# Kernel tuning notes

Hardware: AMD Instinct MI355X
Metric: run time of the kernel (lower is better)

The kernel has to match this reference:

```python
import jax, jax.numpy as jnp
import numpy as np

B, S, HID = 1, 1024, 4096
H, D = 32, 128
KB, NUM_SLOTS, KB_IDX = 2048, 2, 0
TOPK = 100
THETA = 10000.0
KB_SCALE = 100.0
NEG = -1e9


def _rope(x, pos):
    # x: [B,H,S,D], pos: [B,S]
    inv = 1.0 / (THETA ** (jnp.arange(0, D, 2, dtype=jnp.float32) / D))
    freqs = pos[..., None].astype(jnp.float32) * inv          # [B,S,D/2]
    emb = jnp.concatenate([freqs, freqs], -1)                  # [B,S,D]
    cos = jnp.cos(emb)[:, None]                                # [B,1,S,D]
    sin = jnp.sin(emb)[:, None]
    x1, x2 = jnp.split(x, 2, -1)
    rot = jnp.concatenate([-x2, x1], -1)
    return x * cos + rot * sin


def setup_inputs() -> dict:
    key = jax.random.key(0)
    ks = jax.random.split(key, 8)
    hidden_states = jax.random.normal(ks[0], (B, S, HID), jnp.float32)
    # standard additive causal mask (0 on allowed, large negative above diagonal)
    causal = jnp.tril(jnp.ones((S, S), bool))
    attention_mask = jnp.where(causal, 0.0, NEG).astype(jnp.float32)[None, None]
    position_ids = jnp.arange(S, dtype=jnp.int64 if jax.config.jax_enable_x64 else jnp.int32)[None].astype(jnp.int32)
    kb_keys = jax.random.normal(ks[1], (KB, NUM_SLOTS * HID), jnp.float32)
    kb_values = jax.random.normal(ks[2], (KB, NUM_SLOTS * HID), jnp.float32)
    std = 0.02
    Wq = jax.random.normal(ks[3], (HID, HID), jnp.float32) * std
    Wq2 = jax.random.normal(ks[4], (HID, HID), jnp.float32) * std
    Wk = jax.random.normal(ks[5], (HID, HID), jnp.float32) * std
    Wv = jax.random.normal(ks[6], (HID, HID), jnp.float32) * std
    Wo = jax.random.normal(ks[7], (HID, HID), jnp.float32) * std
    score_shift = jnp.zeros((H, 1), jnp.float32) - 3.0
    return dict(hidden_states=hidden_states, attention_mask=attention_mask,
                position_ids=position_ids, kb_keys=kb_keys, kb_values=kb_values,
                Wq=Wq, Wq2=Wq2, Wk=Wk, Wv=Wv, Wo=Wo, score_shift=score_shift)


def reference(hidden_states, attention_mask, position_ids, kb_keys, kb_values,
              Wq, Wq2, Wk, Wv, Wo, score_shift):
    b, s, _ = hidden_states.shape
    heads = lambda x: x.reshape(b, s, H, D).transpose(0, 2, 1, 3)
    q = heads(hidden_states @ Wq.T)
    q2 = heads(hidden_states @ Wq2.T)
    k = heads(hidden_states @ Wk.T)
    v = heads(hidden_states @ Wv.T)
    q = _rope(q, position_ids)
    k = _rope(k, position_ids)
    scale = 1.0 / jnp.sqrt(jnp.asarray(D, jnp.float32))

    # ---- KB branch (2-dim kb_kvs, layer_idx % kb_layer_frequency == 0) ----
    kbk = kb_keys.reshape(KB, NUM_SLOTS, HID)[:, KB_IDX].reshape(KB, H, D).transpose(1, 0, 2)  # [H,KB,D]
    kbv = kb_values.reshape(KB, NUM_SLOTS, HID)[:, KB_IDX].reshape(KB, H, D).transpose(1, 0, 2)
    kbk = jnp.broadcast_to(kbk[None], (b, H, KB, D))
    kbv = jnp.broadcast_to(kbv[None], (b, H, KB, D))

    # dynamic_sparsify: top-k pruning of KB entries by summed q2-scores
    aw2_full = jnp.einsum('bhqd,bhkd->bhqk', q2, kbk) * scale     # [b,H,S,KB]
    kb_scores = jax.lax.stop_gradient(aw2_full.sum((1, 2)))       # [b,KB]
    _, top_idx = jax.lax.top_k(kb_scores, TOPK)                   # [b,TOPK]
    gather = jax.vmap(lambda a, i: a[:, i])                        # [H,KB,D],[TOPK]->[H,TOPK,D]
    kbk_t = gather(kbk, top_idx)
    kbv_t = gather(kbv, top_idx)

    keys = jnp.concatenate([kbk_t, k], 2)                         # [b,H,TOPK+S,D]
    vals = jnp.concatenate([kbv_t, v], 2)

    aw = jnp.einsum('bhqd,bhkd->bhqk', q, keys) * scale           # [b,H,S,TOPK+S]

    # sep_query_head: KB logits use q2, per-head score_shift, log scale-factor correction
    aw2 = jnp.einsum('bhqd,bhkd->bhqk', q2, kbk_t) * scale        # [b,H,S,TOPK]
    aw2 = aw2 + score_shift.reshape(1, H, 1, 1)
    aw2 = aw2 - jnp.log(jnp.asarray(TOPK, jnp.float32)) + jnp.log(jnp.asarray(KB_SCALE, jnp.float32))
    aw = jnp.concatenate([aw2, aw[..., TOPK:]], -1)

    # mask: KB columns fully visible (no fully-padded rows in causal mask)
    kb_mask = jnp.zeros((b, 1, s, TOPK), attention_mask.dtype)
    mask = jnp.concatenate([kb_mask, attention_mask], -1)
    probs = jax.nn.softmax((aw + mask).astype(jnp.float32), -1).astype(q.dtype)

    out = jnp.einsum('bhqk,bhkd->bhqd', probs, vals)
    out = out.transpose(0, 2, 1, 3).reshape(b, s, HID)
    return out @ Wo.T
```

## Files before the change

kernel.cpp:

```cpp
#include <hip/hip_runtime.h>
#include <hip/hip_bf16.h>
#include <math.h>

typedef __hip_bfloat16 bf16_t;
typedef __attribute__((ext_vector_type(8))) short short8;
typedef __attribute__((ext_vector_type(4))) float f32x4;

#define S_LEN 1024
#define HID   4096
#define NH    32
#define HD    128
#define KB_N  2048
#define TOPK  100
#define SCALE 0.08838834764831845f

typedef const __attribute__((address_space(1))) void* gptr_t;
typedef __attribute__((address_space(3))) void* lptr_t;

#define VM8 asm volatile("s_waitcnt vmcnt(8)" ::: "memory")
#define VM4 asm volatile("s_waitcnt vmcnt(4)" ::: "memory")
#define VM0 asm volatile("s_waitcnt vmcnt(0)" ::: "memory")

__global__ void k0_zero(float* __restrict__ out, float* __restrict__ hssum) {
  int tid = threadIdx.x;
  if (blockIdx.x < 4096) {
    float4 z = {0.f, 0.f, 0.f, 0.f};
    *(float4*)(out + ((size_t)blockIdx.x * 256 + tid) * 4) = z;
  } else {
    float4 z = {0.f, 0.f, 0.f, 0.f};
    *(float4*)(hssum + tid * 4) = z;
    *(float4*)(hssum + 1024 + tid * 4) = z;
    *(float4*)(hssum + 2048 + tid * 4) = z;
    *(float4*)(hssum + 3072 + tid * 4) = z;
  }
}

__global__ void kw_conv(const float* __restrict__ Wq, const float* __restrict__ Wq2,
                        const float* __restrict__ Wk, const float* __restrict__ Wv,
                        const float* __restrict__ Wo,
                        bf16_t* __restrict__ Wcat, bf16_t* __restrict__ Wob) {
  int w = blockIdx.y;
  const float* src = (w == 0) ? Wq : (w == 1) ? Wq2 : (w == 2) ? Wk : (w == 3) ? Wv : Wo;
  bf16_t* dst = (w < 4) ? (Wcat + (size_t)w * 16777216) : Wob;
  size_t i = ((size_t)blockIdx.x * 256 + threadIdx.x) * 4;
  float4 f = *(const float4*)(src + i);
  union { bf16_t h[4]; uint2 u; } p;
  p.h[0] = __float2bfloat16(f.x); p.h[1] = __float2bfloat16(f.y);
  p.h[2] = __float2bfloat16(f.z); p.h[3] = __float2bfloat16(f.w);
  *(uint2*)(dst + i) = p.u;
}

__global__ void k1_convert(const float* __restrict__ hs, bf16_t* __restrict__ hsb) {
  size_t i = ((size_t)blockIdx.x * 256 + threadIdx.x) * 4;
  float4 f = *(const float4*)(hs + i);
  union { bf16_t h[4]; uint2 u; } p;
  p.h[0] = __float2bfloat16(f.x); p.h[1] = __float2bfloat16(f.y);
  p.h[2] = __float2bfloat16(f.z); p.h[3] = __float2bfloat16(f.w);
  *(uint2*)(hsb + i) = p.u;
}

__global__ void k1_colsum(const float* __restrict__ hs, float* __restrict__ hssum) {
  int col = blockIdx.x * 256 + threadIdx.x;
  int r0 = blockIdx.y * 64;
  float acc = 0.f;
#pragma unroll 8
  for (int r = 0; r < 64; r++) acc += hs[(size_t)(r0 + r) * HID + col];
  atomicAdd(hssum + col, acc);
}

__global__ void k2_q2sum(const float* __restrict__ W,
                         const float* __restrict__ hssum,
                         float* __restrict__ q2sum) {
  int wave = threadIdx.x >> 6, lane = threadIdx.x & 63;
  int row = blockIdx.x * 4 + wave;
  const float4* wr = (const float4*)(W + (size_t)row * HID);
  const float4* xr = (const float4*)hssum;
  float acc = 0.f;
#pragma unroll
  for (int it = 0; it < 16; it++) {
    float4 a = wr[it * 64 + lane];
    float4 b = xr[it * 64 + lane];
    acc += a.x * b.x + a.y * b.y + a.z * b.z + a.w * b.w;
  }
#pragma unroll
  for (int off = 32; off > 0; off >>= 1) acc += __shfl_xor(acc, off, 64);
  if (lane == 0) q2sum[row] = acc;
}

__global__ void k3_kbscore(const float* __restrict__ kbk,
                           const float* __restrict__ q2sum,
                           float* __restrict__ scores) {
  int wave = threadIdx.x >> 6, lane = threadIdx.x & 63;
  int row = blockIdx.x * 4 + wave;
  const float4* kr = (const float4*)(kbk + (size_t)row * 8192);
  const float4* xr = (const float4*)q2sum;
  float acc = 0.f;
#pragma unroll
  for (int it = 0; it < 16; it++) {
    float4 a = kr[it * 64 + lane];
    float4 b = xr[it * 64 + lane];
    acc += a.x * b.x + a.y * b.y + a.z * b.z + a.w * b.w;
  }
#pragma unroll
  for (int off = 32; off > 0; off >>= 1) acc += __shfl_xor(acc, off, 64);
  if (lane == 0) scores[row] = acc * SCALE;
}

__global__ void k4_topk(const float* __restrict__ scores, int* __restrict__ tidx) {
  int lane = threadIdx.x;
  float v[32];
#pragma unroll
  for (int i = 0; i < 32; i++) v[i] = scores[i * 64 + lane];
  for (int t = 0; t < TOPK; t++) {
    float bm = -INFINITY; int bi = 0x7fffffff;
#pragma unroll
    for (int i = 0; i < 32; i++) {
      if (v[i] > bm) { bm = v[i]; bi = i * 64 + lane; }
    }
#pragma unroll
    for (int off = 32; off > 0; off >>= 1) {
      float ov = __shfl_xor(bm, off, 64);
      int   oi = __shfl_xor(bi, off, 64);
      if (ov > bm || (ov == bm && oi < bi)) { bm = ov; bi = oi; }
    }
    if (lane == 0) tidx[t] = bi;
    if ((bi & 63) == lane) {
      int slot = bi >> 6;
#pragma unroll
      for (int i = 0; i < 32; i++) if (i == slot) v[i] = -INFINITY;
    }
  }
}

__global__ void k5_gather(const float* __restrict__ kbk, const float* __restrict__ kbv,
                          const int* __restrict__ tidx,
                          bf16_t* __restrict__ kbkt, bf16_t* __restrict__ kbvt) {
  int j = blockIdx.x;
  int tid = threadIdx.x;
  if (j < TOPK) {
    size_t src = (size_t)tidx[j] * 8192;
#pragma unroll
    for (int r = 0; r < 4; r++) {
      int i = (tid + r * 256) * 4;
      float4 a = *(const float4*)(kbk + src + i);
      float4 b = *(const float4*)(kbv + src + i);
      union { bf16_t h[4]; uint2 u; } pa, pb;
      pa.h[0] = __float2bfloat16(a.x); pa.h[1] = __float2bfloat16(a.y);
      pa.h[2] = __float2bfloat16(a.z); pa.h[3] = __float2bfloat16(a.w);
      pb.h[0] = __float2bfloat16(b.x); pb.h[1] = __float2bfloat16(b.y);
      pb.h[2] = __float2bfloat16(b.z); pb.h[3] = __float2bfloat16(b.w);
      *(uint2*)(kbkt + (size_t)j * HID + i) = pa.u;
      *(uint2*)(kbvt + (size_t)j * HID + i) = pb.u;
    }
  } else {
    uint2 z; z.x = 0u; z.y = 0u;
#pragma unroll
    for (int r = 0; r < 4; r++) {
      int i = (tid + r * 256) * 4;
      *(uint2*)(kbkt + (size_t)j * HID + i) = z;
      *(uint2*)(kbvt + (size_t)j * HID + i) = z;
    }
  }
}

template<int MODE>
__global__ __launch_bounds__(512, 2) void gemm_256(
    const bf16_t* __restrict__ A, const bf16_t* __restrict__ B,
    void* O0, void* O1, void* O2, void* O3) {
  __shared__ __attribute__((aligned(16))) bf16_t sm[4 * 16384];
  const int tid  = threadIdx.x;
  const int wave = tid >> 6, lane = tid & 63;
  const int lrow = lane & 15, quad = lane >> 4;
  const int wr = wave >> 2, wc = wave & 3;
  const int bm = blockIdx.y * 256;
  const int bn = blockIdx.x * 256;
  const int srow = tid >> 2;
  const int lc   = (tid & 3) ^ ((srow >> 1) & 3);
  const int pc   = quad ^ ((lrow >> 1) & 3);

  const int kbeg = (MODE == 1) ? blockIdx.z * 1024 : 0;
  const int NT   = (MODE == 1) ? 32 : 128;

  const bf16_t* aS = A + (size_t)(bm + srow) * 4096 + kbeg + lc * 8;
  const bf16_t* bS = B + (size_t)(bn + srow) * 4096 + kbeg + lc * 8;
  bf16_t* const lw = sm + wave * 512;

  f32x4 acc[8][4];
  const f32x4 zero4 = {0.f, 0.f, 0.f, 0.f};
#pragma unroll
  for (int i = 0; i < 8; i++)
#pragma unroll
    for (int j = 0; j < 4; j++) acc[i][j] = zero4;

  auto STAGE = [&](int tt) {
    bf16_t* l = lw + (tt & 3) * 16384;
    const bf16_t* ga = aS + tt * 32;
    const bf16_t* gb = bS + tt * 32;
    __builtin_amdgcn_global_load_lds((gptr_t)ga,             (lptr_t)l,           16, 0, 0);
    __builtin_amdgcn_global_load_lds((gptr_t)(ga + 524288),  (lptr_t)(l + 4096),  16, 0, 0);
    __builtin_amdgcn_global_load_lds((gptr_t)gb,             (lptr_t)(l + 8192),  16, 0, 0);
    __builtin_amdgcn_global_load_lds((gptr_t)(gb + 524288),  (lptr_t)(l + 12288), 16, 0, 0);
  };

  STAGE(0); STAGE(1); STAGE(2);
  VM8;
  __builtin_amdgcn_s_barrier();

  auto body = [&](int t, bool do_stage) {
    const bf16_t* Ab = sm + (t & 3) * 16384 + (wr * 128 + lrow) * 32 + pc * 8;
    const bf16_t* Bb = sm + (t & 3) * 16384 + 8192 + (wc * 64 + lrow) * 32 + pc * 8;
    if (do_stage) STAGE(t + 3);
    short8 af[4], bfr[4];
#pragma unroll
    for (int j = 0; j < 4; j++) bfr[j] = *(const short8*)(Bb + j * 512);
#pragma unroll
    for (int i = 0; i < 4; i++) af[i] = *(const short8*)(Ab + i * 512);
    __builtin_amdgcn_s_setprio(1);
#pragma unroll
    for (int i = 0; i < 4; i++)
#pragma unroll
      for (int j = 0; j < 4; j++)
        acc[i][j] = __builtin_amdgcn_mfma_f32_16x16x32_bf16(af[i], bfr[j], acc[i][j], 0, 0, 0);
    __builtin_amdgcn_s_setprio(0);
#pragma unroll
    for (int i = 0; i < 4; i++) af[i] = *(const short8*)(Ab + (i + 4) * 512);
    __builtin_amdgcn_s_setprio(1);
#pragma unroll
    for (int i = 0; i < 4; i++)
#pragma unroll
      for (int j = 0; j < 4; j++)
        acc[i + 4][j] = __builtin_amdgcn_mfma_f32_16x16x32_bf16(af[i], bfr[j], acc[i + 4][j], 0, 0, 0);
    __builtin_amdgcn_s_setprio(0);
  };

  for (int t = 0; t < NT - 3; ++t) {
    body(t, true);
    VM8;
    __builtin_amdgcn_s_barrier();
  }
  body(NT - 3, false); VM4; __builtin_amdgcn_s_barrier();
  body(NT - 2, false); VM0; __builtin_amdgcn_s_barrier();
  body(NT - 1, false);

  if (MODE == 0) {
    bf16_t* dst = (bf16_t*)((bn >> 12) == 0 ? O0 : (bn >> 12) == 1 ? O1
                          : (bn >> 12) == 2 ? O2 : O3);
    const int nb = bn & 4095;
#pragma unroll
    for (int i = 0; i < 8; i++)
#pragma unroll
      for (int j = 0; j < 4; j++)
#pragma unroll
        for (int r = 0; r < 4; r++) {
          int m = bm + wr * 128 + i * 16 + quad * 4 + r;
          int n = nb + wc * 64 + j * 16 + lrow;
          dst[(size_t)m * 4096 + n] = __float2bfloat16(acc[i][j][r]);
        }
  } else {
    float* dst = (float*)O0;
#pragma unroll
    for (int i = 0; i < 8; i++)
#pragma unroll
      for (int j = 0; j < 4; j++)
#pragma unroll
        for (int r = 0; r < 4; r++) {
          int m = bm + wr * 128 + i * 16 + quad * 4 + r;
          int n = bn + wc * 64 + j * 16 + lrow;
          atomicAdd(dst + (size_t)m * 4096 + n, acc[i][j][r]);
        }
  }
}

template<int OUT_BF16>
__global__ __launch_bounds__(256) void gemm_bt(
    const bf16_t* __restrict__ A,
    const float* __restrict__ B0, const float* __restrict__ B1,
    const float* __restrict__ B2, const float* __restrict__ B3,
    void* C0, void* C1, void* C2, void* C3) {
  const int z = blockIdx.z;
  const float* __restrict__ B = (z == 0) ? B0 : (z == 1) ? B1 : (z == 2) ? B2 : B3;
  void* Cv = (z == 0) ? C0 : (z == 1) ? C1 : (z == 2) ? C2 : C3;
  __shared__ bf16_t As[128][40];
  __shared__ bf16_t Bs[128][40];
  const int tid = threadIdx.x;
  const int bm = blockIdx.y * 128, bn = blockIdx.x * 128;
  const int wave = tid >> 6, lane = tid & 63;
  const int wr = wave >> 1, wc = wave & 1;
  const int lrow = lane & 15, quad = lane >> 4;
  f32x4 acc[4][4];
  const f32x4 zero4 = {0.f, 0.f, 0.f, 0.f};
#pragma unroll
  for (int i = 0; i < 4; i++)
#pragma unroll
    for (int j = 0; j < 4; j++) acc[i][j] = zero4;
  const int arow = tid >> 2, ach = tid & 3;
  const int brow = tid >> 3, bch = tid & 7;
  for (int k0 = 0; k0 < 4096; k0 += 32) {
    __syncthreads();
#pragma unroll
    for (int r = 0; r < 2; r++) {
      int row = arow + r * 64;
      uint4 val = *(const uint4*)(A + (size_t)(bm + row) * 4096 + k0 + ach * 8);
      *(uint4*)(&As[row][ach * 8]) = val;
    }
#pragma unroll
    for (int r = 0; r < 4; r++) {
      int row = brow + r * 32;
      float4 f = *(const float4*)(B + (size_t)(bn + row) * 4096 + k0 + bch * 4);
      union { bf16_t h[4]; uint2 u; } p;
      p.h[0] = __float2bfloat16(f.x); p.h[1] = __float2bfloat16(f.y);
      p.h[2] = __float2bfloat16(f.z); p.h[3] = __float2bfloat16(f.w);
      *(uint2*)(&Bs[row][bch * 4]) = p.u;
    }
    __syncthreads();
    short8 af[4], bfr[4];
#pragma unroll
    for (int i = 0; i < 4; i++)
      af[i] = *(const short8*)(&As[wr * 64 + i * 16 + lrow][quad * 8]);
#pragma unroll
    for (int j = 0; j < 4; j++)
      bfr[j] = *(const short8*)(&Bs[wc * 64 + j * 16 + lrow][quad * 8]);
#pragma unroll
    for (int i = 0; i < 4; i++)
#pragma unroll
      for (int j = 0; j < 4; j++)
        acc[i][j] = __builtin_amdgcn_mfma_f32_16x16x32_bf16(af[i], bfr[j], acc[i][j], 0, 0, 0);
  }
#pragma unroll
  for (int i = 0; i < 4; i++)
#pragma unroll
    for (int j = 0; j < 4; j++)
#pragma unroll
      for (int r = 0; r < 4; r++) {
        int m = bm + wr * 64 + i * 16 + quad * 4 + r;
        int n = bn + wc * 64 + j * 16 + lrow;
        if (OUT_BF16)
          ((bf16_t*)Cv)[(size_t)m * 4096 + n] = __float2bfloat16(acc[i][j][r]);
        else
          ((float*)Cv)[(size_t)m * 4096 + n] = acc[i][j][r];
      }
}

__global__ void k7_rope(bf16_t* __restrict__ q, bf16_t* __restrict__ k,
                        const int* __restrict__ pos_ids) {
  int t = blockIdx.x * 256 + threadIdx.x;
  int d = t & 63;
  int h = (t >> 6) & 31;
  int s = t >> 11;
  float pos = (float)pos_ids[s];
  float inv = exp2f(-(float)d * 0.20762050593046f);
  float ang = pos * inv;
  float c = cosf(ang), si = sinf(ang);
  size_t i1 = (size_t)s * HID + h * HD + d;
  size_t i2 = i1 + 64;
  float a1 = __bfloat162float(q[i1]), a2 = __bfloat162float(q[i2]);
  q[i1] = __float2bfloat16(a1 * c - a2 * si);
  q[i2] = __float2bfloat16(a2 * c + a1 * si);
  float b1 = __bfloat162float(k[i1]), b2 = __bfloat162float(k[i2]);
  k[i1] = __float2bfloat16(b1 * c - b2 * si);
  k[i2] = __float2bfloat16(b2 * c + b1 * si);
}

#define FA_PAD 136
__global__ __launch_bounds__(256) void k8_flash(
    const bf16_t* __restrict__ qg, const bf16_t* __restrict__ q2g,
    const bf16_t* __restrict__ kg, const bf16_t* __restrict__ vg,
    const bf16_t* __restrict__ kbkt, const bf16_t* __restrict__ kbvt,
    const float* __restrict__ shift_p,
    bf16_t* __restrict__ outb) {
  __shared__ bf16_t KV[128][FA_PAD];
  __shared__ bf16_t Ps[4][16][FA_PAD];
  int qt = 15 - (int)blockIdx.x;
  int h = blockIdx.y;
  int q0 = qt * 64;
  int tid = threadIdx.x;
  int wave = tid >> 6, lane = tid & 63;
  int lrow = lane & 15, quad = lane >> 4;

  short8 qf[4], q2f[4];
  {
    const size_t base = (size_t)(q0 + wave * 16 + lrow) * HID + h * HD;
#pragma unroll
    for (int kc = 0; kc < 4; kc++) {
      qf[kc]  = *(const short8*)(qg  + base + kc * 32 + quad * 8);
      q2f[kc] = *(const short8*)(q2g + base + kc * 32 + quad * 8);
    }
  }
  const f32x4 zero4 = {0.f, 0.f, 0.f, 0.f};
  f32x4 O[8];
#pragma unroll
  for (int df = 0; df < 8; df++) O[df] = zero4;
  float m_i[4], l_i[4];
#pragma unroll
  for (int r = 0; r < 4; r++) { m_i[r] = -INFINITY; l_i[r] = 0.f; }
  float shift = shift_p[h];

  int nt = (q0 + 63) / 128 + 1;
  for (int tile = -1; tile < nt; tile++) {
    const bf16_t* ksrc = (tile < 0) ? (kbkt + h * HD)
                                    : (kg + (size_t)tile * 128 * HID + h * HD);
    const bf16_t* vsrc = (tile < 0) ? (kbvt + h * HD)
                                    : (vg + (size_t)tile * 128 * HID + h * HD);
    __syncthreads();
    {
      int rbase = tid >> 4, ch = tid & 15;
#pragma unroll
      for (int rr = 0; rr < 8; rr++) {
        int row = rr * 16 + rbase;
        uint4 val = *(const uint4*)(ksrc + (size_t)row * HID + ch * 8);
        *(uint4*)(&KV[row][ch * 8]) = val;
      }
    }
    __syncthreads();
    f32x4 Sv[8];
#pragma unroll
    for (int jf = 0; jf < 8; jf++) {
      short8 kf[4];
#pragma unroll
      for (int kc = 0; kc < 4; kc++)
        kf[kc] = *(const short8*)(&KV[jf * 16 + lrow][kc * 32 + quad * 8]);
      f32x4 s = zero4;
      if (tile < 0) {
#pragma unroll
        for (int kc = 0; kc < 4; kc++)
          s = __builtin_amdgcn_mfma_f32_16x16x32_bf16(q2f[kc], kf[kc], s, 0, 0, 0);
      } else {
#pragma unroll
        for (int kc = 0; kc < 4; kc++)
          s = __builtin_amdgcn_mfma_f32_16x16x32_bf16(qf[kc], kf[kc], s, 0, 0, 0);
      }
      Sv[jf] = s;
    }
#pragma unroll
    for (int jf = 0; jf < 8; jf++)
#pragma unroll
      for (int r = 0; r < 4; r++) {
        float val = Sv[jf][r] * SCALE;
        if (tile < 0) {
          val += shift;
          int col = jf * 16 + lrow;
          if (col >= TOPK) val = -1e30f;
        } else {
          int srow = q0 + wave * 16 + quad * 4 + r;
          int tcol = tile * 128 + jf * 16 + lrow;
          if (tcol > srow) val -= 1e9f;
        }
        Sv[jf][r] = val;
      }
    float alpha[4];
#pragma unroll
    for (int r = 0; r < 4; r++) {
      float tm = Sv[0][r];
#pragma unroll
      for (int jf = 1; jf < 8; jf++) tm = fmaxf(tm, Sv[jf][r]);
#pragma unroll
      for (int off = 1; off < 16; off <<= 1) tm = fmaxf(tm, __shfl_xor(tm, off, 64));
      float mn = fmaxf(m_i[r], tm);
      alpha[r] = __expf(m_i[r] - mn);
      m_i[r] = mn;
    }
    float rsum[4] = {0.f, 0.f, 0.f, 0.f};
#pragma unroll
    for (int jf = 0; jf < 8; jf++)
#pragma unroll
      for (int r = 0; r < 4; r++) {
        float p = __expf(Sv[jf][r] - m_i[r]);
        Sv[jf][r] = p;
        rsum[r] += p;
      }
#pragma unroll
    for (int r = 0; r < 4; r++) {
#pragma unroll
      for (int off = 1; off < 16; off <<= 1) rsum[r] += __shfl_xor(rsum[r], off, 64);
      l_i[r] = l_i[r] * alpha[r] + rsum[r];
    }
#pragma unroll
    for (int jf = 0; jf < 8; jf++)
#pragma unroll
      for (int r = 0; r < 4; r++)
        Ps[wave][quad * 4 + r][jf * 16 + lrow] = __float2bfloat16(Sv[jf][r]);
#pragma unroll
    for (int df = 0; df < 8; df++)
#pragma unroll
      for (int r = 0; r < 4; r++) O[df][r] *= alpha[r];
    __syncthreads();
    {
      int rbase = tid >> 4, ch = tid & 15;
#pragma unroll
      for (int rr = 0; rr < 8; rr++) {
        int t = rr * 16 + rbase;
        union { uint4 u; bf16_t hx[8]; } vv;
        vv.u = *(const uint4*)(vsrc + (size_t)t * HID + ch * 8);
        int cs = ((t >> 3) ^ ch) & 15;
        int tl = t & 7;
#pragma unroll
        for (int e = 0; e < 8; e++)
          KV[ch * 8 + e][cs * 8 + tl] = vv.hx[e];
      }
    }
    __syncthreads();
    short8 pf[4];
#pragma unroll
    for (int kc = 0; kc < 4; kc++)
      pf[kc] = *(const short8*)(&Ps[wave][lrow][kc * 32 + quad * 8]);
#pragma unroll
    for (int df = 0; df < 8; df++) {
      int d = df * 16 + lrow;
      int sw = (d >> 3) & 15;
#pragma unroll
      for (int kc = 0; kc < 4; kc++) {
        short8 vf = *(const short8*)(&KV[d][(((kc * 4 + quad) ^ sw) & 15) * 8]);
        O[df] = __builtin_amdgcn_mfma_f32_16x16x32_bf16(pf[kc], vf, O[df], 0, 0, 0);
      }
    }
  }
#pragma unroll
  for (int df = 0; df < 8; df++)
#pragma unroll
    for (int r = 0; r < 4; r++) {
      int srow = q0 + wave * 16 + quad * 4 + r;
      float val = O[df][r] / l_i[r];
      outb[(size_t)srow * HID + h * HD + df * 16 + lrow] = __float2bfloat16(val);
    }
}

extern "C" void kernel_launch(void* const* d_in, const int* in_sizes, int n_in,
                              void* d_out, int out_size, void* d_ws, size_t ws_size,
                              hipStream_t stream) {
  const float* hs    = (const float*)d_in[0];
  const int*   pos   = (const int*)d_in[2];
  const float* kbk   = (const float*)d_in[3];
  const float* kbv   = (const float*)d_in[4];
  const float* Wq    = (const float*)d_in[5];
  const float* Wq2   = (const float*)d_in[6];
  const float* Wk    = (const float*)d_in[7];
  const float* Wv    = (const float*)d_in[8];
  const float* Wo    = (const float*)d_in[9];
  const float* shift = (const float*)d_in[10];
  float* out = (float*)d_out;

  char* ws = (char*)d_ws;
  const size_t MB8 = 8388608;
  bf16_t* qb    = (bf16_t*)(ws);
  bf16_t* q2b   = (bf16_t*)(ws + MB8);
  bf16_t* kbuf  = (bf16_t*)(ws + 2 * MB8);
  bf16_t* vbuf  = (bf16_t*)(ws + 3 * MB8);
  bf16_t* hsb   = (bf16_t*)(ws + 4 * MB8);
  bf16_t* kbkt  = (bf16_t*)(ws + 5 * MB8);
  bf16_t* kbvt  = (bf16_t*)(ws + 5 * MB8 + 1048576);
  float*  hssum = (float*)(ws + 5 * MB8 + 2 * 1048576);
  float*  q2s   = (float*)(ws + 5 * MB8 + 2 * 1048576 + 16384);
  float*  scr   = (float*)(ws + 5 * MB8 + 2 * 1048576 + 32768);
  int*    tidx  = (int*)(ws + 5 * MB8 + 2 * 1048576 + 40960);
  bf16_t* attnb = hsb;
  const size_t WCAT_OFF = 48ull * 1048576;
  bf16_t* Wcat = (bf16_t*)(ws + WCAT_OFF);
  bf16_t* Wob  = (bf16_t*)(ws + WCAT_OFF + 134217728);
  const size_t WS_NEED = WCAT_OFF + 134217728 + 33554432;
  const bool big_ws = (ws_size >= WS_NEED);

  k0_zero<<<dim3(4097), dim3(256), 0, stream>>>(out, hssum);
  if (big_ws)
    kw_conv<<<dim3(16384, 5), dim3(256), 0, stream>>>(Wq, Wq2, Wk, Wv, Wo, Wcat, Wob);
  k1_convert<<<dim3(4096), dim3(256), 0, stream>>>(hs, hsb);
  k1_colsum<<<dim3(16, 16), dim3(256), 0, stream>>>(hs, hssum);
  k2_q2sum<<<dim3(1024), dim3(256), 0, stream>>>(Wq2, hssum, q2s);
  k3_kbscore<<<dim3(512), dim3(256), 0, stream>>>(kbk, q2s, scr);
  k4_topk<<<dim3(1), dim3(64), 0, stream>>>(scr, tidx);
  k5_gather<<<dim3(128), dim3(256), 0, stream>>>(kbk, kbv, tidx, kbkt, kbvt);

  if (big_ws) {
    gemm_256<0><<<dim3(64, 4), dim3(512), 0, stream>>>(
        hsb, Wcat, (void*)qb, (void*)q2b, (void*)kbuf, (void*)vbuf);
  } else {
    gemm_bt<1><<<dim3(32, 8, 4), dim3(256), 0, stream>>>(
        hsb, Wq, Wq2, Wk, Wv, (void*)qb, (void*)q2b, (void*)kbuf, (void*)vbuf);
  }
  k7_rope<<<dim3(8192), dim3(256), 0, stream>>>(qb, kbuf, pos);
  k8_flash<<<dim3(16, 32), dim3(256), 0, stream>>>(
      qb, q2b, kbuf, vbuf, kbkt, kbvt, shift, attnb);
  if (big_ws) {
    gemm_256<1><<<dim3(16, 4, 4), dim3(512), 0, stream>>>(
        attnb, Wob, (void*)out, nullptr, nullptr, nullptr);
  } else {
    gemm_bt<0><<<dim3(32, 8, 1), dim3(256), 0, stream>>>(
        attnb, Wo, Wo, Wo, Wo, (void*)out, (void*)out, (void*)out, (void*)out);
  }
}
```

Measured before the change: 809.8 us.

## Double-buffer MFMA fragments in projection GEMM; replace split-K atomic Wo GEMM

Measured after the change: 758.7 us. -6.3%, faster.

```diff
diff --git a/kernel.cpp b/kernel.cpp
--- a/kernel.cpp
+++ b/kernel.cpp
@@ -17,22 +17,16 @@
 typedef const __attribute__((address_space(1))) void* gptr_t;
 typedef __attribute__((address_space(3))) void* lptr_t;
 
-#define VM8 asm volatile("s_waitcnt vmcnt(8)" ::: "memory")
 #define VM4 asm volatile("s_waitcnt vmcnt(4)" ::: "memory")
 #define VM0 asm volatile("s_waitcnt vmcnt(0)" ::: "memory")
 
-__global__ void k0_zero(float* __restrict__ out, float* __restrict__ hssum) {
+__global__ void k0_zero(float* __restrict__ hssum) {
   int tid = threadIdx.x;
-  if (blockIdx.x < 4096) {
-    float4 z = {0.f, 0.f, 0.f, 0.f};
-    *(float4*)(out + ((size_t)blockIdx.x * 256 + tid) * 4) = z;
-  } else {
-    float4 z = {0.f, 0.f, 0.f, 0.f};
-    *(float4*)(hssum + tid * 4) = z;
-    *(float4*)(hssum + 1024 + tid * 4) = z;
-    *(float4*)(hssum + 2048 + tid * 4) = z;
-    *(float4*)(hssum + 3072 + tid * 4) = z;
-  }
+  float4 z = {0.f, 0.f, 0.f, 0.f};
+  *(float4*)(hssum + tid * 4) = z;
+  *(float4*)(hssum + 1024 + tid * 4) = z;
+  *(float4*)(hssum + 2048 + tid * 4) = z;
+  *(float4*)(hssum + 3072 + tid * 4) = z;
 }
 
 __global__ void kw_conv(const float* __restrict__ Wq, const float* __restrict__ Wq2,
@@ -163,8 +157,7 @@
   }
 }
 
-template<int MODE>
-__global__ __launch_bounds__(512, 2) void gemm_256(
+__global__ __launch_bounds__(512, 2) void gemm_proj(
     const bf16_t* __restrict__ A, const bf16_t* __restrict__ B,
     void* O0, void* O1, void* O2, void* O3) {
   __shared__ __attribute__((aligned(16))) bf16_t sm[4 * 16384];
@@ -178,11 +171,8 @@
   const int lc   = (tid & 3) ^ ((srow >> 1) & 3);
   const int pc   = quad ^ ((lrow >> 1) & 3);
 
-  const int kbeg = (MODE == 1) ? blockIdx.z * 1024 : 0;
-  const int NT   = (MODE == 1) ? 32 : 128;
-
-  const bf16_t* aS = A + (size_t)(bm + srow) * 4096 + kbeg + lc * 8;
-  const bf16_t* bS = B + (size_t)(bn + srow) * 4096 + kbeg + lc * 8;
+  const bf16_t* aS = A + (size_t)(bm + srow) * 4096 + lc * 8;
+  const bf16_t* bS = B + (size_t)(bn + srow) * 4096 + lc * 8;
   bf16_t* const lw = sm + wave * 512;
 
   f32x4 acc[8][4];
@@ -202,73 +192,176 @@
     __builtin_amdgcn_global_load_lds((gptr_t)(gb + 524288),  (lptr_t)(l + 12288), 16, 0, 0);
   };
 
+  short8 fa0[4], fb0[4], fa1[4], fb1[4], afB[4];
+
+  auto body = [&](int t, short8 (&FAC)[4], short8 (&FBC)[4],
+                  short8 (&FAN)[4], short8 (&FBN)[4],
+                  bool pf, bool stg, int vmn, bool barr) {
+    const bf16_t* Ab = sm + (t & 3) * 16384 + (wr * 128 + lrow) * 32 + pc * 8;
+    if (stg) STAGE(t + 3);
+#pragma unroll
+    for (int i = 0; i < 4; i++) afB[i] = *(const short8*)(Ab + (i + 4) * 512);
+    __builtin_amdgcn_s_setprio(1);
+#pragma unroll
+    for (int i = 0; i < 4; i++)
+#pragma unroll
+      for (int j = 0; j < 4; j++)
+        acc[i][j] = __builtin_amdgcn_mfma_f32_16x16x32_bf16(FAC[i], FBC[j], acc[i][j], 0, 0, 0);
+    __builtin_amdgcn_s_setprio(0);
+    if (pf) {
+      const bf16_t* An = sm + ((t + 1) & 3) * 16384 + (wr * 128 + lrow) * 32 + pc * 8;
+      const bf16_t* Bn = sm + ((t + 1) & 3) * 16384 + 8192 + (wc * 64 + lrow) * 32 + pc * 8;
+#pragma unroll
+      for (int j = 0; j < 4; j++) FBN[j] = *(const short8*)(Bn + j * 512);
+#pragma unroll
+      for (int i = 0; i < 4; i++) FAN[i] = *(const short8*)(An + i * 512);
+    }
+    __builtin_amdgcn_s_setprio(1);
+#pragma unroll
+    for (int i = 0; i < 4; i++)
+#pragma unroll
+      for (int j = 0; j < 4; j++)
+        acc[i + 4][j] = __builtin_amdgcn_mfma_f32_16x16x32_bf16(afB[i], FBC[j], acc[i + 4][j], 0, 0, 0);
+    __builtin_amdgcn_s_setprio(0);
+    if (vmn == 4) { VM4; }
+    else if (vmn == 0) { VM0; }
+    if (barr) __builtin_amdgcn_s_barrier();
+  };
+
   STAGE(0); STAGE(1); STAGE(2);
-  VM8;
+  VM4;
   __builtin_amdgcn_s_barrier();
-
-  auto body = [&](int t, bool do_stage) {
-    const bf16_t* Ab = sm + (t & 3) * 16384 + (wr * 128 + lrow) * 32 + pc * 8;
-    const bf16_t* Bb = sm + (t & 3) * 16384 + 8192 + (wc * 64 + lrow) * 32 + pc * 8;
-    if (do_stage) STAGE(t + 3);
-    short8 af[4], bfr[4];
-#pragma unroll
-    for (int j = 0; j < 4; j++) bfr[j] = *(const short8*)(Bb + j * 512);
-#pragma unroll
-    for (int i = 0; i < 4; i++) af[i] = *(const short8*)(Ab + i * 512);
+  {
+    const bf16_t* Ab = sm + (wr * 128 + lrow) * 32 + pc * 8;
+    const bf16_t* Bb = sm + 8192 + (wc * 64 + lrow) * 32 + pc * 8;
+#pragma unroll
+    for (int j = 0; j < 4; j++) fb0[j] = *(const short8*)(Bb + j * 512);
+#pragma unroll
+    for (int i = 0; i < 4; i++) fa0[i] = *(const short8*)(Ab + i * 512);
+  }
+
+  for (int t = 0; t < 124; t += 2) {
+    body(t,     fa0, fb0, fa1, fb1, true, true, 4, true);
+    body(t + 1, fa1, fb1, fa0, fb0, true, true, 4, true);
+  }
+  body(124, fa0, fb0, fa1, fb1, true,  true,  4, true);
+  body(125, fa1, fb1, fa0, fb0, true,  false, 0, true);
+  body(126, fa0, fb0, fa1, fb1, true,  false, -1, false);
+  body(127, fa1, fb1, fa0, fb0, false, false, -1, false);
+
+  bf16_t* dst = (bf16_t*)((bn >> 12) == 0 ? O0 : (bn >> 12) == 1 ? O1
+                        : (bn >> 12) == 2 ? O2 : O3);
+  const int nb = bn & 4095;
+#pragma unroll
+  for (int i = 0; i < 8; i++)
+#pragma unroll
+    for (int j = 0; j < 4; j++)
+#pragma unroll
+      for (int r = 0; r < 4; r++) {
+        int m = bm + wr * 128 + i * 16 + quad * 4 + r;
+        int n = nb + wc * 64 + j * 16 + lrow;
+        dst[(size_t)m * 4096 + n] = __float2bfloat16(acc[i][j][r]);
+      }
+}
+
+__global__ __launch_bounds__(512, 2) void gemm_wo(
+    const bf16_t* __restrict__ A, const bf16_t* __restrict__ B,
+    float* __restrict__ out) {
+  __shared__ __attribute__((aligned(16))) bf16_t sm[4 * 16384];
+  const int tid  = threadIdx.x;
+  const int wave = tid >> 6, lane = tid & 63;
+  const int lrow = lane & 15, quad = lane >> 4;
+  const int wrr = wave >> 2, wcc = wave & 3;
+  const int bm = blockIdx.y * 128;
+  const int bn = blockIdx.x * 128;
+  const int srow8 = lane >> 3;
+  const int lcw   = (lane & 7) ^ srow8;
+  const int grp   = (wave & 3) * 32;
+  const bf16_t* wS = ((wave < 4) ? A + (size_t)(bm + grp + srow8) * 4096
+                                 : B + (size_t)(bn + grp + srow8) * 4096) + lcw * 8;
+  bf16_t* const lw = sm + (wave < 4 ? 0 : 8192) + grp * 64;
+  const int pcw0 = ((quad)     ^ (lrow & 7)) * 8;
+  const int pcw1 = ((4 + quad) ^ (lrow & 7)) * 8;
+
+  f32x4 acc[4][2];
+  const f32x4 zero4 = {0.f, 0.f, 0.f, 0.f};
+#pragma unroll
+  for (int i = 0; i < 4; i++)
+#pragma unroll
+    for (int j = 0; j < 2; j++) acc[i][j] = zero4;
+
+  auto STAGE = [&](int tt) {
+    bf16_t* l = lw + (tt & 3) * 16384;
+    const bf16_t* g = wS + tt * 64;
+    __builtin_amdgcn_global_load_lds((gptr_t)g,              (lptr_t)l,           16, 0, 0);
+    __builtin_amdgcn_global_load_lds((gptr_t)(g + 32768),    (lptr_t)(l + 512),   16, 0, 0);
+    __builtin_amdgcn_global_load_lds((gptr_t)(g + 65536),    (lptr_t)(l + 1024),  16, 0, 0);
+    __builtin_amdgcn_global_load_lds((gptr_t)(g + 98304),    (lptr_t)(l + 1536),  16, 0, 0);
+  };
+
+  short8 ga0[8], gb0[4], ga1[8], gb1[4];
+
+  auto rdfrag = [&](int t, short8 (&GA)[8], short8 (&GB)[4]) {
+    const bf16_t* An = sm + (t & 3) * 16384;
+    const bf16_t* Bn = An + 8192;
+#pragma unroll
+    for (int n = 0; n < 2; n++) {
+      int row = wcc * 32 + n * 16 + lrow;
+      GB[n * 2]     = *(const short8*)(Bn + row * 64 + pcw0);
+      GB[n * 2 + 1] = *(const short8*)(Bn + row * 64 + pcw1);
+    }
+#pragma unroll
+    for (int m = 0; m < 4; m++) {
+      int row = wrr * 64 + m * 16 + lrow;
+      GA[m * 2]     = *(const short8*)(An + row * 64 + pcw0);
+      GA[m * 2 + 1] = *(const short8*)(An + row * 64 + pcw1);
+    }
+  };
+
+  auto body = [&](int t, short8 (&GA)[8], short8 (&GB)[4],
+                  short8 (&NA)[8], short8 (&NB)[4],
+                  bool pf, bool stg, int vmn, bool barr) {
+    if (stg) STAGE(t + 3);
+    if (pf) rdfrag(t + 1, NA, NB);
     __builtin_amdgcn_s_setprio(1);
 #pragma unroll
-    for (int i = 0; i < 4; i++)
-#pragma unroll
-      for (int j = 0; j < 4; j++)
-        acc[i][j] = __builtin_amdgcn_mfma_f32_16x16x32_bf16(af[i], bfr[j], acc[i][j], 0, 0, 0);
+    for (int kk = 0; kk < 2; kk++)
+#pragma unroll
+      for (int m = 0; m < 4; m++)
+#pragma unroll
+        for (int n = 0; n < 2; n++)
+          acc[m][n] = __builtin_amdgcn_mfma_f32_16x16x32_bf16(
+              GA[m * 2 + kk], GB[n * 2 + kk], acc[m][n], 0, 0, 0);
     __builtin_amdgcn_s_setprio(0);
-#pragma unroll
-    for (int i = 0; i < 4; i++) af[i] = *(const short8*)(Ab + (i + 4) * 512);
-    __builtin_amdgcn_s_setprio(1);
-#pragma unroll
-    for (int i = 0; i < 4; i++)
-#pragma unroll
-      for (int j = 0; j < 4; j++)
-        acc[i + 4][j] = __builtin_amdgcn_mfma_f32_16x16x32_bf16(af[i], bfr[j], acc[i + 4][j], 0, 0, 0);
-    __builtin_amdgcn_s_setprio(0);
+    if (vmn == 4) { VM4; }
+    else if (vmn == 0) { VM0; }
+    if (barr) __builtin_amdgcn_s_barrier();
   };
 
-  for (int t = 0; t < NT - 3; ++t) {
-    body(t, true);
-    VM8;
-    __builtin_amdgcn_s_barrier();
-  }
-  body(NT - 3, false); VM4; __builtin_amdgcn_s_barrier();
-  body(NT - 2, false); VM0; __builtin_amdgcn_s_barrier();
-  body(NT - 1, false);
-
-  if (MODE == 0) {
-    bf16_t* dst = (bf16_t*)((bn >> 12) == 0 ? O0 : (bn >> 12) == 1 ? O1
-                          : (bn >> 12) == 2 ? O2 : O3);
-    const int nb = bn & 4095;
-#pragma unroll
-    for (int i = 0; i < 8; i++)
-#pragma unroll
-      for (int j = 0; j < 4; j++)
-#pragma unroll
-        for (int r = 0; r < 4; r++) {
-          int m = bm + wr * 128 + i * 16 + quad * 4 + r;
-          int n = nb + wc * 64 + j * 16 + lrow;
-          dst[(size_t)m * 4096 + n] = __float2bfloat16(acc[i][j][r]);
-        }
-  } else {
-    float* dst = (float*)O0;
-#pragma unroll
-    for (int i = 0; i < 8; i++)
-#pragma unroll
-      for (int j = 0; j < 4; j++)
-#pragma unroll
-        for (int r = 0; r < 4; r++) {
-          int m = bm + wr * 128 + i * 16 + quad * 4 + r;
-          int n = bn + wc * 64 + j * 16 + lrow;
-          atomicAdd(dst + (size_t)m * 4096 + n, acc[i][j][r]);
-        }
-  }
+  STAGE(0); STAGE(1); STAGE(2);
+  VM4;
+  __builtin_amdgcn_s_barrier();
+  rdfrag(0, ga0, gb0);
+
+  for (int t = 0; t < 60; t += 2) {
+    body(t,     ga0, gb0, ga1, gb1, true, true, 4, true);
+    body(t + 1, ga1, gb1, ga0, gb0, true, true, 4, true);
+  }
+  body(60, ga0, gb0, ga1, gb1, true,  true,  4, true);
+  body(61, ga1, gb1, ga0, gb0, true,  false, 0, true);
+  body(62, ga0, gb0, ga1, gb1, true,  false, -1, false);
+  body(63, ga1, gb1, ga0, gb0, false, false, -1, false);
+
+#pragma unroll
+  for (int m = 0; m < 4; m++)
+#pragma unroll
+    for (int n = 0; n < 2; n++)
+#pragma unroll
+      for (int r = 0; r < 4; r++) {
+        int row = bm + wrr * 64 + m * 16 + quad * 4 + r;
+        int col = bn + wcc * 32 + n * 16 + lrow;
+        out[(size_t)row * 4096 + col] = acc[m][n][r];
+      }
 }
 
 template<int OUT_BF16>
@@ -559,7 +652,7 @@
   const size_t WS_NEED = WCAT_OFF + 134217728 + 33554432;
   const bool big_ws = (ws_size >= WS_NEED);
 
-  k0_zero<<<dim3(4097), dim3(256), 0, stream>>>(out, hssum);
+  k0_zero<<<dim3(1), dim3(256), 0, stream>>>(hssum);
   if (big_ws)
     kw_conv<<<dim3(16384, 5), dim3(256), 0, stream>>>(Wq, Wq2, Wk, Wv, Wo, Wcat, Wob);
   k1_convert<<<dim3(4096), dim3(256), 0, stream>>>(hs, hsb);
@@ -570,7 +663,7 @@
   k5_gather<<<dim3(128), dim3(256), 0, stream>>>(kbk, kbv, tidx, kbkt, kbvt);
 
   if (big_ws) {
-    gemm_256<0><<<dim3(64, 4), dim3(512), 0, stream>>>(
+    gemm_proj<<<dim3(64, 4), dim3(512), 0, stream>>>(
         hsb, Wcat, (void*)qb, (void*)q2b, (void*)kbuf, (void*)vbuf);
   } else {
     gemm_bt<1><<<dim3(32, 8, 4), dim3(256), 0, stream>>>(
@@ -580,8 +673,7 @@
   k8_flash<<<dim3(16, 32), dim3(256), 0, stream>>>(
       qb, q2b, kbuf, vbuf, kbkt, kbvt, shift, attnb);
   if (big_ws) {
-    gemm_256<1><<<dim3(16, 4, 4), dim3(512), 0, stream>>>(
-        attnb, Wob, (void*)out, nullptr, nullptr, nullptr);
+    gemm_wo<<<dim3(32, 8), dim3(512), 0, stream>>>(attnb, Wob, out);
   } else {
     gemm_bt<0><<<dim3(32, 8, 1), dim3(256), 0, stream>>>(
         attnb, Wo, Wo, Wo, Wo, (void*)out, (void*)out, (void*)out, (void*)out);
```
